# Kernel tuning notes

Measured on AMD Instinct MI355X. Metric: run time of the kernel, lower is better.

## Reference

```python
import jax, jax.numpy as jnp
import numpy as np


def setup_inputs() -> dict:
    key = jax.random.key(0)
    k1, k2, k3, k4 = jax.random.split(key, 4)
    B, N, M, D = 4, 8192, 8192, 3
    pred = jax.random.normal(k1, (B, N, D), dtype=jnp.float32)
    target = jax.random.normal(k2, (B, M, D), dtype=jnp.float32)
    bpp = jax.random.uniform(k3, (), dtype=jnp.float32)
    lamda = jax.random.uniform(k4, (), dtype=jnp.float32)
    return {"pred": pred, "target": target, "bpp": bpp, "lamda": lamda}


def _chamfer(pred, target):
    # pred: [B, N, 3], target: [B, M, 3]
    # squared pairwise distances: [B, N, M]
    diff = pred[:, :, None, :] - target[:, None, :, :]
    d2 = jnp.sum(diff * diff, axis=-1)
    cham_x = jnp.min(d2, axis=2).mean(axis=1)  # [B] pred -> target
    cham_y = jnp.min(d2, axis=1).mean(axis=1)  # [B] target -> pred
    return (cham_x + cham_y).mean()  # batch-mean of summed directions (pytorch3d default)


def reference(pred, target, bpp, lamda):
    dist = _chamfer(pred, target)
    return dist + lamda * bpp
```

## Files before the change

kernel.cpp:

```cpp
#include <hip/hip_runtime.h>

#define NPTS 8192
#define NB 4

#define WPB 8
#define ITILES 4
#define ROWS_PER_WAVE (ITILES * 16)
#define ROWS_PER_BLOCK (WPB * ROWS_PER_WAVE)
#define CHUNK 512
#define JT (CHUNK / 16)
#define CHUNKS (NPTS / CHUNK)
#define ROWBLKS (NPTS / ROWS_PER_BLOCK)

using bf16x8 = __attribute__((ext_vector_type(8))) short;
using f32x4  = __attribute__((ext_vector_type(4))) float;

__device__ __forceinline__ unsigned short bfb(float v) {
    unsigned int x = __float_as_uint(v);
    return (unsigned short)((x + 0x7FFFu + ((x >> 16) & 1u)) >> 16);
}
__device__ __forceinline__ float bff(unsigned short u) {
    return __uint_as_float(((unsigned int)u) << 16);
}
__device__ __forceinline__ void split3(float v, unsigned short& H,
                                       unsigned short& M, unsigned short& L) {
    H = bfb(v); float r = v - bff(H);
    M = bfb(r); L = bfb(r - bff(M));
}
__device__ __forceinline__ unsigned int pk(unsigned short lo, unsigned short hi) {
    return (unsigned int)lo | ((unsigned int)hi << 16);
}
__device__ __forceinline__ unsigned int umn(unsigned int a, unsigned int b) {
    return a < b ? a : b;
}

__device__ __forceinline__ void encA(float x, float y, float z, char* base) {
    const unsigned short ONE = 0x3F80u;
    float pp = fmaf(x, x, fmaf(y, y, z * z));
    unsigned short xH,xM,xL, yH,yM,yL, zH,zM,zL, pH,pM,pL;
    split3(-2.f * x, xH, xM, xL);
    split3(-2.f * y, yH, yM, yL);
    split3(-2.f * z, zH, zM, zL);
    split3(pp, pH, pM, pL);
    uint4 q0 = make_uint4(pk(xH,xH), pk(xM,xH), pk(xL,xM), pk(yH,yH));
    uint4 q1 = make_uint4(pk(yM,yH), pk(yL,yM), pk(zH,zH), pk(zM,zH));
    uint4 q2 = make_uint4(pk(zL,zM), pk(pH,pM), pk(pL,ONE), pk(ONE,ONE));
    uint4 q3 = make_uint4(0u, 0u, 0u, 0u);
    *(uint4*)(base +   0) = q0;
    *(uint4*)(base + 256) = q1;
    *(uint4*)(base + 512) = q2;
    *(uint4*)(base + 768) = q3;
}
__device__ __forceinline__ void encB(float x, float y, float z, char* base) {
    const unsigned short ONE = 0x3F80u;
    float pp = fmaf(x, x, fmaf(y, y, z * z));
    unsigned short xH,xM,xL, yH,yM,yL, zH,zM,zL, pH,pM,pL;
    split3(x, xH, xM, xL);
    split3(y, yH, yM, yL);
    split3(z, zH, zM, zL);
    split3(pp, pH, pM, pL);
    uint4 q0 = make_uint4(pk(xH,xM), pk(xH,xL), pk(xH,xM), pk(yH,yM));
    uint4 q1 = make_uint4(pk(yH,yL), pk(yH,yM), pk(zH,zM), pk(zH,zL));
    uint4 q2 = make_uint4(pk(zH,zM), pk(ONE,ONE), pk(ONE,pH), pk(pM,pL));
    *(uint4*)(base +   0) = q0;
    *(uint4*)(base + 256) = q1;
    *(uint4*)(base + 512) = q2;
}

__device__ __forceinline__ void tile_pair(
    const bf16x8 (&af)[ITILES], bf16x8 b0, bf16x8 b1,
    f32x4 (&rmin)[ITILES], unsigned int* colh, int cbase,
    const f32x4& zf)
{
    f32x4 cp0 = {3e38f, 3e38f, 3e38f, 3e38f};
    f32x4 cp1 = {3e38f, 3e38f, 3e38f, 3e38f};
#pragma unroll
    for (int it = 0; it < ITILES; it += 2) {
        f32x4 d00 = __builtin_amdgcn_mfma_f32_16x16x32_bf16(af[it],     b0, zf, 0, 0, 0);
        f32x4 d01 = __builtin_amdgcn_mfma_f32_16x16x32_bf16(af[it],     b1, zf, 0, 0, 0);
        f32x4 d10 = __builtin_amdgcn_mfma_f32_16x16x32_bf16(af[it + 1], b0, zf, 0, 0, 0);
        f32x4 d11 = __builtin_amdgcn_mfma_f32_16x16x32_bf16(af[it + 1], b1, zf, 0, 0, 0);
#pragma unroll
        for (int r = 0; r < 4; ++r) {
            rmin[it][r]     = fminf(fminf(d00[r], d01[r]), rmin[it][r]);
            rmin[it + 1][r] = fminf(fminf(d10[r], d11[r]), rmin[it + 1][r]);
            cp0[r]          = fminf(fminf(d00[r], d10[r]), cp0[r]);
            cp1[r]          = fminf(fminf(d01[r], d11[r]), cp1[r]);
        }
    }
    float c0 = fminf(fminf(cp0[0], cp0[1]), fminf(cp0[2], cp0[3]));
    float c1 = fminf(fminf(cp1[0], cp1[1]), fminf(cp1[2], cp1[3]));
    c0 = fmaxf(c0, 0.f);
    c1 = fmaxf(c1, 0.f);
    atomicMin(&colh[cbase],      __float_as_uint(c0));
    atomicMin(&colh[cbase + 64], __float_as_uint(c1));
}

__global__ __launch_bounds__(512, 6) void chamfer_fused(
    const float* __restrict__ pred, const float* __restrict__ target,
    float* __restrict__ rowpart, float* __restrict__ colpart,
    float* __restrict__ out, const float* __restrict__ bpp,
    const float* __restrict__ lamda)
{
    __shared__ short bB[JT * 512];
    __shared__ unsigned int colh[CHUNK * 4];

    const int tid  = threadIdx.x;
    const int lane = tid & 63;
    const int w    = tid >> 6;
    const int bid  = blockIdx.x;
    const int ck   = bid & (CHUNKS - 1);
    const int rb   = (bid >> 4) & (ROWBLKS - 1);
    const int b    = bid >> 8;

    const int col0 = ck * CHUNK;
    const float* asrc = pred   + (size_t)b * NPTS * 3;
    const float* bsrc = target + (size_t)b * NPTS * 3;

    const int ag = rb * ROWS_PER_BLOCK + tid;
    float ax = asrc[3 * ag + 0], ay = asrc[3 * ag + 1], az = asrc[3 * ag + 2];
    const int bg = col0 + tid;
    float bx = bsrc[3 * bg + 0], by = bsrc[3 * bg + 1], bz = bsrc[3 * bg + 2];

    if (bid == 0 && tid == 0) out[0] = lamda[0] * bpp[0];

    for (int i = tid; i < CHUNK * 4; i += 512) colh[i] = 0x7F7F7F7Fu;

    encA(ax, ay, az,
         (char*)bB + w * 4096 + (lane >> 4) * 1024 + (lane & 15) * 16);

    bf16x8 af[ITILES];
    {
        const char* ab = (const char*)bB + w * 4096 + lane * 16;
#pragma unroll
        for (int it = 0; it < ITILES; ++it)
            af[it] = *(const bf16x8*)(ab + it * 1024);
    }
    __syncthreads();

    encB(bx, by, bz, (char*)bB + (tid >> 4) * 1024 + (tid & 15) * 16);

    f32x4 rmin[ITILES];
#pragma unroll
    for (int it = 0; it < ITILES; ++it) {
        rmin[it][0] = 3e38f; rmin[it][1] = 3e38f;
        rmin[it][2] = 3e38f; rmin[it][3] = 3e38f;
    }
    const f32x4 zf = {0.f, 0.f, 0.f, 0.f};

    __syncthreads();

    const char* bb = (const char*)bB + lane * 16;
    bf16x8 B0 = *(const bf16x8*)(bb);
    bf16x8 B1 = *(const bf16x8*)(bb + 1024);
    int cbase = (lane & 15) * 4 + (lane >> 4);
    for (int jt = 0; jt < JT; jt += 2) {
        int nj = (jt + 2) & (JT - 1);
        bf16x8 Bn0 = *(const bf16x8*)(bb + nj * 1024);
        bf16x8 Bn1 = *(const bf16x8*)(bb + (nj + 1) * 1024);
        tile_pair(af, B0, B1, rmin, colh, cbase, zf);
        cbase += 128;
        B0 = Bn0; B1 = Bn1;
    }

    __syncthreads();

    {
        char* sb = (char*)bB + w * 2560;
        const int hi = lane >> 4, col = lane & 15;
#pragma unroll
        for (int p = 0; p < 2; ++p) {
#pragma unroll
            for (int halfit = 0; halfit < 2; ++halfit) {
#pragma unroll
                for (int r = 0; r < 4; ++r) {
                    int row32 = halfit * 16 + hi * 4 + r;
                    *(float*)(sb + row32 * 80 + col * 4) = rmin[p * 2 + halfit][r];
                }
            }
            const int a = lane >> 1, bsel = lane & 1;
            const char* rp = sb + a * 80 + bsel * 32;
            f32x4 v0 = *(const f32x4*)(rp);
            f32x4 v1 = *(const f32x4*)(rp + 16);
            float v = fminf(fminf(fminf(v0[0], v0[1]), fminf(v0[2], v0[3])),
                            fminf(fminf(v1[0], v1[1]), fminf(v1[2], v1[3])));
            v = fminf(v, __shfl_xor(v, 1, 64));
            if (bsel == 0) {
                int row = rb * ROWS_PER_BLOCK + w * ROWS_PER_WAVE + p * 32 + a;
                rowpart[((size_t)(b * CHUNKS) + ck) * NPTS + row] = fmaxf(v, 0.f);
            }
            __builtin_amdgcn_sched_barrier(0);
        }
    }

    for (int i = tid; i < CHUNK; i += 512) {
        uint4 v = *(const uint4*)&colh[i * 4];
        unsigned int m = umn(umn(v.x, v.y), umn(v.z, v.w));
        colpart[((size_t)(b * ROWBLKS) + rb) * NPTS + col0 + i] = __uint_as_float(m);
    }
}

__global__ __launch_bounds__(256) void reduce_partials(
    const float* __restrict__ rowpart, const float* __restrict__ colpart,
    float* __restrict__ out)
{
    const int tid = threadIdx.x;
    const int gt  = blockIdx.x * 256 + tid;
    float s = 0.f;
#pragma unroll
    for (int a = 0; a < 2; a++) {
        const float* P = a ? colpart : rowpart;
#pragma unroll
        for (int cc = 0; cc < 2; cc++) {
            int c = gt + cc * 16384;
            int b = c >> 13, r = c & 8191;
            const float* p = P + (size_t)b * 16 * NPTS + r;
            float m = p[0];
#pragma unroll
            for (int k = 1; k < 16; k++)
                m = fminf(m, p[(size_t)k * NPTS]);
            s += m;
        }
    }
#pragma unroll
    for (int off = 32; off > 0; off >>= 1) s += __shfl_down(s, off, 64);
    __shared__ float red[4];
    int lane = tid & 63, wid = tid >> 6;
    if (lane == 0) red[wid] = s;
    __syncthreads();
    if (tid == 0)
        atomicAdd(out, (red[0] + red[1] + red[2] + red[3]) * (1.0f / 32768.0f));
}

#define T 256
#define Q 8
#define S 16
#define CH 512
#define NCOMBO 8

__global__ __launch_bounds__(T) void chamfer_partial(
    const float* __restrict__ pred, const float* __restrict__ target,
    unsigned int* __restrict__ partmin)
{
    __shared__ float4 db[CH + 2];

    const int bid   = blockIdx.x;
    const int dbc   = bid & (S - 1);
    const int qc    = (bid >> 4) & 3;
    const int combo = bid >> 6;
    const int dir   = combo & 1;
    const int b     = combo >> 1;

    const float* qptr = (dir == 0 ? pred : target) + (size_t)b * NPTS * 3;
    const float* dptr = (dir == 0 ? target : pred) + (size_t)b * NPTS * 3;

    const int tid = threadIdx.x;

    for (int p = tid; p < CH; p += T) {
        int gj = dbc * CH + p;
        float x = dptr[gj * 3 + 0];
        float y = dptr[gj * 3 + 1];
        float z = dptr[gj * 3 + 2];
        db[p] = make_float4(-2.f * x, -2.f * y, -2.f * z,
                            x * x + y * y + z * z);
    }

    float qx[Q], qy[Q], qz[Q], m[Q];
    int qi0 = qc * (T * Q) + tid;
#pragma unroll
    for (int k = 0; k < Q; k++) {
        int qi = qi0 + k * T;
        qx[k] = qptr[qi * 3 + 0];
        qy[k] = qptr[qi * 3 + 1];
        qz[k] = qptr[qi * 3 + 2];
        m[k]  = 3.4e38f;
    }
    __syncthreads();

    float4 c0 = db[0], c1 = db[1];
    for (int j = 0; j < CH; j += 2) {
        float4 n0 = db[j + 2];
        float4 n1 = db[j + 3];
#pragma unroll
        for (int k = 0; k < Q; k++) {
            float s0 = fmaf(c0.x, qx[k], fmaf(c0.y, qy[k], fmaf(c0.z, qz[k], c0.w)));
            float s1 = fmaf(c1.x, qx[k], fmaf(c1.y, qy[k], fmaf(c1.z, qz[k], c1.w)));
            m[k] = fminf(m[k], fminf(s0, s1));
        }
        c0 = n0; c1 = n1;
    }

#pragma unroll
    for (int k = 0; k < Q; k++) {
        int qi = qi0 + k * T;
        float qq = fmaf(qx[k], qx[k], fmaf(qy[k], qy[k], qz[k] * qz[k]));
        float d2 = fmaxf(m[k] + qq, 0.0f);
        atomicMin(&partmin[combo * NPTS + qi], __float_as_uint(d2));
    }
}

__global__ __launch_bounds__(1024) void reduce_final(
    const unsigned int* __restrict__ partmin,
    const float* __restrict__ bpp, const float* __restrict__ lamda,
    float* __restrict__ out)
{
    const int tid = threadIdx.x;
    float s = 0.f;
#pragma unroll
    for (int k = 0; k < (NCOMBO * NPTS) / 1024; k++)
        s += __uint_as_float(partmin[tid + k * 1024]);

#pragma unroll
    for (int off = 32; off > 0; off >>= 1)
        s += __shfl_down(s, off, 64);

    __shared__ float red[16];
    int lane = tid & 63, wid = tid >> 6;
    if (lane == 0) red[wid] = s;
    __syncthreads();
    if (wid == 0) {
        s = (lane < 16) ? red[lane] : 0.f;
#pragma unroll
        for (int off = 8; off > 0; off >>= 1)
            s += __shfl_down(s, off, 64);
        if (lane == 0)
            out[0] = s * (1.0f / 32768.0f) + lamda[0] * bpp[0];
    }
}

extern "C" void kernel_launch(void* const* d_in, const int* in_sizes, int n_in,
                              void* d_out, int out_size, void* d_ws, size_t ws_size,
                              hipStream_t stream) {
    const float* pred   = (const float*)d_in[0];
    const float* target = (const float*)d_in[1];
    const float* bpp    = (const float*)d_in[2];
    const float* lamda  = (const float*)d_in[3];

    const size_t part_bytes = (size_t)NB * 16 * NPTS * sizeof(float);

    if (ws_size >= 2 * part_bytes) {
        float* rowpart = (float*)d_ws;
        float* colpart = rowpart + (size_t)NB * 16 * NPTS;
        chamfer_fused<<<NB * ROWBLKS * CHUNKS, 512, 0, stream>>>(
            pred, target, rowpart, colpart, (float*)d_out, bpp, lamda);
        reduce_partials<<<64, 256, 0, stream>>>(rowpart, colpart, (float*)d_out);
    } else {
        unsigned int* partmin = (unsigned int*)d_ws;
        hipMemsetAsync(partmin, 0x7F, (size_t)NCOMBO * NPTS * sizeof(unsigned int),
                       stream);
        chamfer_partial<<<NCOMBO * 4 * S, T, 0, stream>>>(pred, target, partmin);
        reduce_final<<<1, 1024, 0, stream>>>(partmin, bpp, lamda, (float*)d_out);
    }
}
```

Before: 82.54 us.

## Use two-term bf16 split with 16x16x16 MFMA for distance matmul

Replaces the three-way bf16 split (H/M/L) of coordinates and norms with a two-way split. This shrinks the inner product to 16 bf16 terms, so it can use the smaller 16x16x16 bf16 MFMA when the builtin exists, with a fallback to zero-padded 16x16x32. The shared-memory layout and fragment loads are repacked to match. It halves the MFMA K dimension and the LDS traffic, at the cost of lower precision in the computed squared distances (roughly 16 mantissa bits).

```diff
diff --git a/kernel.cpp b/kernel.cpp
--- a/kernel.cpp
+++ b/kernel.cpp
@@ -12,8 +12,19 @@
 #define CHUNKS (NPTS / CHUNK)
 #define ROWBLKS (NPTS / ROWS_PER_BLOCK)
 
+using bf16x4 = __attribute__((ext_vector_type(4))) short;
 using bf16x8 = __attribute__((ext_vector_type(8))) short;
 using f32x4  = __attribute__((ext_vector_type(4))) float;
+
+#if __has_builtin(__builtin_amdgcn_mfma_f32_16x16x16bf16_1k)
+#define HAVE_MFMA16 1
+typedef bf16x4 afrag;
+#define MFMA_BF16(a, b, c) __builtin_amdgcn_mfma_f32_16x16x16bf16_1k(a, b, c, 0, 0, 0)
+#else
+#define HAVE_MFMA16 0
+typedef bf16x8 afrag;
+#define MFMA_BF16(a, b, c) __builtin_amdgcn_mfma_f32_16x16x32_bf16(a, b, c, 0, 0, 0)
+#endif
 
 __device__ __forceinline__ unsigned short bfb(float v) {
     unsigned int x = __float_as_uint(v);
@@ -22,10 +33,8 @@
 __device__ __forceinline__ float bff(unsigned short u) {
     return __uint_as_float(((unsigned int)u) << 16);
 }
-__device__ __forceinline__ void split3(float v, unsigned short& H,
-                                       unsigned short& M, unsigned short& L) {
-    H = bfb(v); float r = v - bff(H);
-    M = bfb(r); L = bfb(r - bff(M));
+__device__ __forceinline__ void split2(float v, unsigned short& H, unsigned short& M) {
+    H = bfb(v); M = bfb(v - bff(H));
 }
 __device__ __forceinline__ unsigned int pk(unsigned short lo, unsigned short hi) {
     return (unsigned int)lo | ((unsigned int)hi << 16);
@@ -34,41 +43,46 @@
     return a < b ? a : b;
 }
 
-__device__ __forceinline__ void encA(float x, float y, float z, char* base) {
+__device__ __forceinline__ void encA16(float x, float y, float z, char* base) {
     const unsigned short ONE = 0x3F80u;
     float pp = fmaf(x, x, fmaf(y, y, z * z));
-    unsigned short xH,xM,xL, yH,yM,yL, zH,zM,zL, pH,pM,pL;
-    split3(-2.f * x, xH, xM, xL);
-    split3(-2.f * y, yH, yM, yL);
-    split3(-2.f * z, zH, zM, zL);
-    split3(pp, pH, pM, pL);
-    uint4 q0 = make_uint4(pk(xH,xH), pk(xM,xH), pk(xL,xM), pk(yH,yH));
-    uint4 q1 = make_uint4(pk(yM,yH), pk(yL,yM), pk(zH,zH), pk(zM,zH));
-    uint4 q2 = make_uint4(pk(zL,zM), pk(pH,pM), pk(pL,ONE), pk(ONE,ONE));
-    uint4 q3 = make_uint4(0u, 0u, 0u, 0u);
-    *(uint4*)(base +   0) = q0;
-    *(uint4*)(base + 256) = q1;
-    *(uint4*)(base + 512) = q2;
-    *(uint4*)(base + 768) = q3;
-}
-__device__ __forceinline__ void encB(float x, float y, float z, char* base) {
+    unsigned short xH,xM, yH,yM, zH,zM, pH,pM;
+    split2(-2.f * x, xH, xM);
+    split2(-2.f * y, yH, yM);
+    split2(-2.f * z, zH, zM);
+    split2(pp, pH, pM);
+    uint4 q0 = make_uint4(pk(xH,xH), pk(xM,xM), pk(yH,yH), pk(yM,yM));
+    uint4 q1 = make_uint4(pk(zH,zH), pk(zM,zM), pk(pH,pM), pk(ONE,ONE));
+    *(uint4*)(base +  0) = q0;
+    *(uint4*)(base + 16) = q1;
+}
+__device__ __forceinline__ void encB16(float x, float y, float z, char* base) {
     const unsigned short ONE = 0x3F80u;
     float pp = fmaf(x, x, fmaf(y, y, z * z));
-    unsigned short xH,xM,xL, yH,yM,yL, zH,zM,zL, pH,pM,pL;
-    split3(x, xH, xM, xL);
-    split3(y, yH, yM, yL);
-    split3(z, zH, zM, zL);
-    split3(pp, pH, pM, pL);
-    uint4 q0 = make_uint4(pk(xH,xM), pk(xH,xL), pk(xH,xM), pk(yH,yM));
-    uint4 q1 = make_uint4(pk(yH,yL), pk(yH,yM), pk(zH,zM), pk(zH,zL));
-    uint4 q2 = make_uint4(pk(zH,zM), pk(ONE,ONE), pk(ONE,pH), pk(pM,pL));
-    *(uint4*)(base +   0) = q0;
-    *(uint4*)(base + 256) = q1;
-    *(uint4*)(base + 512) = q2;
+    unsigned short xH,xM, yH,yM, zH,zM, pH,pM;
+    split2(x, xH, xM);
+    split2(y, yH, yM);
+    split2(z, zH, zM);
+    split2(pp, pH, pM);
+    unsigned int wx = pk(xH,xM), wy = pk(yH,yM), wz = pk(zH,zM);
+    uint4 q0 = make_uint4(wx, wx, wy, wy);
+    uint4 q1 = make_uint4(wz, wz, pk(ONE,ONE), pk(pH,pM));
+    *(uint4*)(base +  0) = q0;
+    *(uint4*)(base + 16) = q1;
+}
+
+__device__ __forceinline__ afrag ld_frag(const char* rec, int hi) {
+#if HAVE_MFMA16
+    return *(const afrag*)(rec + hi * 8);
+#else
+    if (hi < 2) return *(const afrag*)(rec + hi * 16);
+    afrag z = {0,0,0,0,0,0,0,0};
+    return z;
+#endif
 }
 
 __device__ __forceinline__ void tile_pair(
-    const bf16x8 (&af)[ITILES], bf16x8 b0, bf16x8 b1,
+    const afrag (&af)[ITILES], afrag b0, afrag b1,
     f32x4 (&rmin)[ITILES], unsigned int* colh, int cbase,
     const f32x4& zf)
 {
@@ -76,10 +90,10 @@
     f32x4 cp1 = {3e38f, 3e38f, 3e38f, 3e38f};
 #pragma unroll
     for (int it = 0; it < ITILES; it += 2) {
-        f32x4 d00 = __builtin_amdgcn_mfma_f32_16x16x32_bf16(af[it],     b0, zf, 0, 0, 0);
-        f32x4 d01 = __builtin_amdgcn_mfma_f32_16x16x32_bf16(af[it],     b1, zf, 0, 0, 0);
-        f32x4 d10 = __builtin_amdgcn_mfma_f32_16x16x32_bf16(af[it + 1], b0, zf, 0, 0, 0);
-        f32x4 d11 = __builtin_amdgcn_mfma_f32_16x16x32_bf16(af[it + 1], b1, zf, 0, 0, 0);
+        f32x4 d00 = MFMA_BF16(af[it],     b0, zf);
+        f32x4 d01 = MFMA_BF16(af[it],     b1, zf);
+        f32x4 d10 = MFMA_BF16(af[it + 1], b0, zf);
+        f32x4 d11 = MFMA_BF16(af[it + 1], b1, zf);
 #pragma unroll
         for (int r = 0; r < 4; ++r) {
             rmin[it][r]     = fminf(fminf(d00[r], d01[r]), rmin[it][r]);
@@ -102,7 +116,7 @@
     float* __restrict__ out, const float* __restrict__ bpp,
     const float* __restrict__ lamda)
 {
-    __shared__ short bB[JT * 512];
+    __shared__ short bB[16384];
     __shared__ unsigned int colh[CHUNK * 4];
 
     const int tid  = threadIdx.x;
@@ -126,19 +140,20 @@
 
     for (int i = tid; i < CHUNK * 4; i += 512) colh[i] = 0x7F7F7F7Fu;
 
-    encA(ax, ay, az,
-         (char*)bB + w * 4096 + (lane >> 4) * 1024 + (lane & 15) * 16);
-
-    bf16x8 af[ITILES];
+    encA16(ax, ay, az,
+           (char*)bB + w * 2048 + (lane >> 4) * 512 + (lane & 15) * 32);
+
+    afrag af[ITILES];
     {
-        const char* ab = (const char*)bB + w * 4096 + lane * 16;
+        const char* ab = (const char*)bB + w * 2048 + (lane & 15) * 32;
+        const int hi = lane >> 4;
 #pragma unroll
         for (int it = 0; it < ITILES; ++it)
-            af[it] = *(const bf16x8*)(ab + it * 1024);
-    }
-    __syncthreads();
-
-    encB(bx, by, bz, (char*)bB + (tid >> 4) * 1024 + (tid & 15) * 16);
+            af[it] = ld_frag(ab + it * 512, hi);
+    }
+    __syncthreads();
+
+    encB16(bx, by, bz, (char*)bB + (tid >> 4) * 512 + (tid & 15) * 32);
 
     f32x4 rmin[ITILES];
 #pragma unroll
@@ -150,14 +165,15 @@
 
     __syncthreads();
 
-    const char* bb = (const char*)bB + lane * 16;
-    bf16x8 B0 = *(const bf16x8*)(bb);
-    bf16x8 B1 = *(const bf16x8*)(bb + 1024);
-    int cbase = (lane & 15) * 4 + (lane >> 4);
+    const char* bb = (const char*)bB + (lane & 15) * 32;
+    const int hi = lane >> 4;
+    afrag B0 = ld_frag(bb, hi);
+    afrag B1 = ld_frag(bb + 512, hi);
+    int cbase = (lane & 15) * 4 + hi;
     for (int jt = 0; jt < JT; jt += 2) {
         int nj = (jt + 2) & (JT - 1);
-        bf16x8 Bn0 = *(const bf16x8*)(bb + nj * 1024);
-        bf16x8 Bn1 = *(const bf16x8*)(bb + (nj + 1) * 1024);
+        afrag Bn0 = ld_frag(bb + nj * 512, hi);
+        afrag Bn1 = ld_frag(bb + (nj + 1) * 512, hi);
         tile_pair(af, B0, B1, rmin, colh, cbase, zf);
         cbase += 128;
         B0 = Bn0; B1 = Bn1;
@@ -167,14 +183,14 @@
 
     {
         char* sb = (char*)bB + w * 2560;
-        const int hi = lane >> 4, col = lane & 15;
+        const int hig = lane >> 4, col = lane & 15;
 #pragma unroll
         for (int p = 0; p < 2; ++p) {
 #pragma unroll
             for (int halfit = 0; halfit < 2; ++halfit) {
 #pragma unroll
                 for (int r = 0; r < 4; ++r) {
-                    int row32 = halfit * 16 + hi * 4 + r;
+                    int row32 = halfit * 16 + hig * 4 + r;
                     *(float*)(sb + row32 * 80 + col * 4) = rmin[p * 2 + halfit][r];
                 }
             }
```

New measurement: 80.07 us (median of 2 runs). 1.03x faster.
